# Kernel optimization log

Hardware: AMD Instinct MI355X
Metric: run time of the kernel (lower is better)

The kernel has to match this reference:

```python
import jax, jax.numpy as jnp
import numpy as np

N_NODES = 100000
N_EDGES = 1600000
IN_CH = 32
HID = 128
EDGE_DIM = 16
BN_EPS = 1e-5


def setup_inputs() -> dict:
    key = jax.random.key(0)
    ks = jax.random.split(key, 32)
    f32 = jnp.float32

    def w(k, shape, scale):
        return jax.random.normal(k, shape, dtype=f32) * scale

    inp = {
        'x': w(ks[0], (N_NODES, IN_CH), 1.0),
        'edge_index': jax.random.randint(ks[1], (2, N_EDGES), 0, N_NODES, dtype=jnp.int32),
        'edge_attr': w(ks[2], (N_EDGES, EDGE_DIM), 1.0),
        # layer 0: in=32 -> out=128
        'l0_We': w(ks[3], (EDGE_DIM, IN_CH), 0.1),
        'l0_be': jnp.zeros((IN_CH,), f32),
        'l0_W1': w(ks[4], (IN_CH, HID), 0.1),
        'l0_b1': jnp.zeros((HID,), f32),
        'l0_W2': w(ks[5], (HID, HID), 0.1),
        'l0_b2': jnp.zeros((HID,), f32),
        'l0_gamma': jnp.ones((HID,), f32),
        'l0_beta': jnp.zeros((HID,), f32),
        # layer 1: 128 -> 128
        'l1_We': w(ks[6], (EDGE_DIM, HID), 0.1),
        'l1_be': jnp.zeros((HID,), f32),
        'l1_W1': w(ks[7], (HID, HID), 0.1),
        'l1_b1': jnp.zeros((HID,), f32),
        'l1_W2': w(ks[8], (HID, HID), 0.1),
        'l1_b2': jnp.zeros((HID,), f32),
        'l1_gamma': jnp.ones((HID,), f32),
        'l1_beta': jnp.zeros((HID,), f32),
        # head MLP: hidden -> hidden -> 1
        'head_W1': w(ks[9], (HID, HID), 0.1),
        'head_b1': jnp.zeros((HID,), f32),
        'head_W2': w(ks[10], (HID, 1), 0.1),
        'head_b2': jnp.zeros((1,), f32),
    }
    return inp


def _gnblock(x, src, dst, e, We, be, W1, b1, W2, b2, gamma, beta):
    # GINE-style message passing: gather -> edge message -> scatter-sum
    msg = jax.nn.relu(x[src] + e @ We + be)              # [E, d_in]
    agg = jax.ops.segment_sum(msg, dst, num_segments=N_NODES)  # [N, d_in]
    h = x + agg                                          # GIN combine (eps=0)
    h = jax.nn.relu(h @ W1 + b1) @ W2 + b2               # 2-layer MLP
    # batch norm over the node dimension (use_norm=True)
    mu = jnp.mean(h, axis=0)
    var = jnp.var(h, axis=0)
    h = (h - mu) * jax.lax.rsqrt(var + BN_EPS) * gamma + beta
    return jax.nn.relu(h)


def reference(x, edge_index, edge_attr,
              l0_We, l0_be, l0_W1, l0_b1, l0_W2, l0_b2, l0_gamma, l0_beta,
              l1_We, l1_be, l1_W1, l1_b1, l1_W2, l1_b2, l1_gamma, l1_beta,
              head_W1, head_b1, head_W2, head_b2):
    src, dst = edge_index[0], edge_index[1]
    h = _gnblock(x, src, dst, edge_attr,
                 l0_We, l0_be, l0_W1, l0_b1, l0_W2, l0_b2, l0_gamma, l0_beta)
    h = _gnblock(h, src, dst, edge_attr,
                 l1_We, l1_be, l1_W1, l1_b1, l1_W2, l1_b2, l1_gamma, l1_beta)
    # MLPBlock head + sigmoid -> per-node selection probability [N, 1]
    out = jax.nn.relu(h @ head_W1 + head_b1) @ head_W2 + head_b2
    return jax.nn.sigmoid(out)
```

## Files before the change

### kernel.cpp

```cpp
#include <hip/hip_runtime.h>

#define NN 100000
#define NE 1600000
#define TMAX 193760
#define NRANGES 24220

typedef unsigned int uint32;
typedef unsigned long long ull;
typedef __attribute__((ext_vector_type(8))) short bf16x8;
typedef __attribute__((ext_vector_type(4))) float f32x4;

__device__ __forceinline__ unsigned short f2bf(float f) {
  unsigned int u = __float_as_uint(f);
  unsigned int r = (u + 0x7fffu + ((u >> 16) & 1u)) >> 16;
  return (unsigned short)r;
}
__device__ __forceinline__ float bf2f(unsigned short u) {
  return __uint_as_float(((unsigned int)u) << 16);
}
__device__ __forceinline__ unsigned int pack2(float a, float b) {
  return (unsigned int)f2bf(a) | ((unsigned int)f2bf(b) << 16);
}
__device__ __forceinline__ float row16_sum(float x) {
  x += __int_as_float(__builtin_amdgcn_mov_dpp(__float_as_int(x), 0x128, 0xf, 0xf, false));
  x += __int_as_float(__builtin_amdgcn_mov_dpp(__float_as_int(x), 0x124, 0xf, 0xf, false));
  x += __int_as_float(__builtin_amdgcn_mov_dpp(__float_as_int(x), 0x122, 0xf, 0xf, false));
  x += __int_as_float(__builtin_amdgcn_mov_dpp(__float_as_int(x), 0x121, 0xf, 0xf, false));
  return x;
}

__device__ __forceinline__ void wconv_body(const float* __restrict__ src,
    unsigned short* __restrict__ dst, int K, int N, int b)
{
  const int i = b * 256 + threadIdx.x;
  if (i < K * N) {
    const int n = i / K, k = i - n * K;
    dst[i] = f2bf(src[k * N + n]);
  }
}

__global__ __launch_bounds__(256) void conv_all(
    const float* __restrict__ l0W1, const float* __restrict__ l0W2,
    const float* __restrict__ l1W1, const float* __restrict__ l1W2,
    const float* __restrict__ hW1,  const float* __restrict__ l0We,
    const float* __restrict__ l1We, const float* __restrict__ x,
    unsigned short* __restrict__ W1t0, unsigned short* __restrict__ W2t0,
    unsigned short* __restrict__ W1t1, unsigned short* __restrict__ W2t1,
    unsigned short* __restrict__ hW1t, unsigned short* __restrict__ Wet0,
    unsigned short* __restrict__ Wet1, unsigned short* __restrict__ xb)
{
  int b = blockIdx.x;
  if (b < 16)  { wconv_body(l0W1, W1t0, 32, 128, b); return; }  b -= 16;
  if (b < 64)  { wconv_body(l0W2, W2t0, 128, 128, b); return; } b -= 64;
  if (b < 64)  { wconv_body(l1W1, W1t1, 128, 128, b); return; } b -= 64;
  if (b < 64)  { wconv_body(l1W2, W2t1, 128, 128, b); return; } b -= 64;
  if (b < 64)  { wconv_body(hW1,  hW1t, 128, 128, b); return; } b -= 64;
  if (b < 2)   { wconv_body(l0We, Wet0, 16, 32, b); return; }   b -= 2;
  if (b < 8)   { wconv_body(l1We, Wet1, 16, 128, b); return; }  b -= 8;
  const int i = b * 256 + threadIdx.x;
  if (i * 8 < NN * 32) {
    const float4 a = ((const float4*)x)[i * 2];
    const float4 d = ((const float4*)x)[i * 2 + 1];
    uint4 o;
    o.x = pack2(a.x, a.y); o.y = pack2(a.z, a.w);
    o.z = pack2(d.x, d.y); o.w = pack2(d.z, d.w);
    ((uint4*)xb)[i] = o;
  }
}

__global__ __launch_bounds__(256) void hist_kernel(
    const int* __restrict__ ei, uint32* __restrict__ deg)
{
  const int e = blockIdx.x * 256 + threadIdx.x;
  if (e < NE) atomicAdd(&deg[ei[NE + e]], 1u);
}

__global__ __launch_bounds__(256) void offsets2_kernel(
    const uint32* __restrict__ deg, uint32* __restrict__ toff,
    uint32* __restrict__ eoff, ull* __restrict__ counter)
{
  __shared__ ull s[256];
  __shared__ ull base;
  const int tid = threadIdx.x;
  const int n = blockIdx.x * 256 + tid;
  const uint32 d = (n < NN) ? deg[n] : 0u;
  const uint32 tc = (d + 15u) >> 4;
  const ull v = ((ull)tc << 32) | (ull)d;
  s[tid] = v;
  __syncthreads();
#pragma unroll
  for (int st = 1; st < 256; st <<= 1) {
    ull w = (tid >= st) ? s[tid - st] : 0ull;
    __syncthreads();
    s[tid] += w;
    __syncthreads();
  }
  if (tid == 255) base = atomicAdd(counter, s[255]);
  __syncthreads();
  if (n < NN) {
    const ull t = base + (s[tid] - v);
    toff[n] = (uint32)(t >> 32);
    eoff[n] = (uint32)t;
  }
}

__global__ __launch_bounds__(256) void snode_fill(
    const uint32* __restrict__ toff, const uint32* __restrict__ deg,
    int* __restrict__ snode)
{
  const int n = blockIdx.x * 256 + threadIdx.x;
  if (n < NN) {
    const uint32 t0 = toff[n];
    const uint32 tc = (deg[n] + 15u) >> 4;
    for (uint32 i = 0; i < tc; ++i) snode[t0 + i] = n;
  }
}

template<bool EAB>
__global__ __launch_bounds__(256) void fill_kernel(
    const int* __restrict__ ei, const uint32* __restrict__ eoff,
    uint32* __restrict__ cnt, uint32* __restrict__ srcc,
    unsigned short* __restrict__ eabc, uint32* __restrict__ eidc,
    const float* __restrict__ ea)
{
  const int e = blockIdx.x * 256 + threadIdx.x;
  if (e < NE) {
    const int dst = ei[NE + e];
    const uint32 pos = eoff[dst] + atomicAdd(&cnt[dst], 1u);
    srcc[pos] = (uint32)ei[e];
    if constexpr (EAB) {
      const float4* er = (const float4*)(ea + (size_t)e * 16);
      const float4 p0 = er[0], p1 = er[1], p2 = er[2], p3 = er[3];
      uint4 lo, hi;
      lo.x = pack2(p0.x, p0.y); lo.y = pack2(p0.z, p0.w);
      lo.z = pack2(p1.x, p1.y); lo.w = pack2(p1.z, p1.w);
      hi.x = pack2(p2.x, p2.y); hi.y = pack2(p2.z, p2.w);
      hi.z = pack2(p3.x, p3.y); hi.w = pack2(p3.z, p3.w);
      *(uint4*)&eabc[(size_t)pos * 16]     = lo;
      *(uint4*)&eabc[(size_t)pos * 16 + 8] = hi;
    } else {
      eidc[pos] = (uint32)e;
    }
  }
}

template<int D, int NCT>
__global__ __launch_bounds__(256) void flat_agg2(
    const int* __restrict__ snode, const uint32* __restrict__ toff,
    const uint32* __restrict__ eoff, const uint32* __restrict__ deg,
    const uint32* __restrict__ srcc, const unsigned short* __restrict__ eabc,
    const unsigned short* __restrict__ hsrc,
    const unsigned short* __restrict__ Wet, const float* __restrict__ be,
    const ull* __restrict__ tot, float* __restrict__ agg)
{
  const int tid = threadIdx.x;
  const int wid = tid >> 6;
  const int lane = tid & 63;
  const int c = lane & 15;
  const int g = lane >> 4;
  constexpr bool HALF = (NCT * 16 != D);
  int range, ch0;
  if (HALF) { range = blockIdx.x * 2 + (wid >> 1); ch0 = (wid & 1) * (NCT * 16); }
  else      { range = blockIdx.x * 4 + wid;        ch0 = 0; }
  const int tile0 = range * 8;
  const uint32 ntile = (uint32)((*tot) >> 32);
  if ((uint32)tile0 >= ntile) return;

  bf16x8 wf[NCT];
#pragma unroll
  for (int ct = 0; ct < NCT; ++ct) {
    const int chA = ch0 + (c >> 2) * (NCT * 4) + ct * 4 + (c & 3);
    uint4 u = make_uint4(0u, 0u, 0u, 0u);
    if (g < 2) u = *(const uint4*)&Wet[chA * 16 + g * 8];
    else if (g == 2) u.x = (uint32)f2bf(be[chA]);
    union { uint4 u4; bf16x8 v; } cv; cv.u4 = u;
    wf[ct] = cv.v;
  }

  int sn8 = -1, pk8 = 0, p_ = 0;
  if (lane < 8) {
    sn8 = snode[tile0 + lane];
    if (sn8 >= 0) {
      const uint32 to = toff[sn8], dg = deg[sn8], eo = eoff[sn8];
      const int k = tile0 + lane - (int)to;
      p_ = (int)eo + k * 16;
      int rv = (int)dg - k * 16; if (rv > 16) rv = 16;
      const int fl = (k == 0 ? 1 : 0) |
                     ((k == (int)((dg + 15u) >> 4) - 1) ? 2 : 0);
      pk8 = (rv << 7) | (fl << 12);
    }
  }
  const int p0base = __shfl(p_, 0);
  if (lane < 8 && sn8 >= 0) pk8 |= (p_ - p0base);

  const uint32 sl0 = srcc[(size_t)p0base + lane];
  const uint32 sl1 = srcc[(size_t)p0base + 64 + lane];

  float acc[NCT][4];
#pragma unroll
  for (int ct = 0; ct < NCT; ++ct) {
    acc[ct][0] = 0.f; acc[ct][1] = 0.f; acc[ct][2] = 0.f; acc[ct][3] = 0.f;
  }
  int openNode = -1; bool openFull = false, openClosed = false;

  auto flushOpen = [&](bool storeOK) {
#pragma unroll
    for (int ct = 0; ct < NCT; ++ct)
#pragma unroll
      for (int j = 0; j < 4; ++j)
        acc[ct][j] = row16_sum(acc[ct][j]);
    float4 sv = make_float4(0.f, 0.f, 0.f, 0.f);
#pragma unroll
    for (int ct = 0; ct < NCT; ++ct)
      if (c == ct)
        sv = make_float4(acc[ct][0], acc[ct][1], acc[ct][2], acc[ct][3]);
    if (c < NCT) {
      float* p = &agg[(size_t)openNode * D + ch0 + g * (NCT * 4) + c * 4];
      if (storeOK) {
        *(float4*)p = sv;
      } else {
        atomicAdd(p + 0, sv.x); atomicAdd(p + 1, sv.y);
        atomicAdd(p + 2, sv.z); atomicAdd(p + 3, sv.w);
      }
    }
  };

  auto issue = [&](int t, uint4& afu, uint4& h0, uint4& h1, int& n_, int& mt_) {
    n_ = __shfl(sn8, t);
    mt_ = __shfl(pk8, t);
    const int d0 = mt_ & 127;
    const int rem = (mt_ >> 7) & 31;
    const int idx = d0 + ((c < rem) ? c : 0);
    const uint32 v0 = __shfl(sl0, idx & 63);
    const uint32 v1 = __shfl(sl1, idx & 63);
    const int src = (int)((idx & 64) ? v1 : v0);
    if (g < 2) afu = *(const uint4*)&eabc[((size_t)p0base + idx) * 16 + g * 8];
    h0 = *(const uint4*)&hsrc[(size_t)src * D + ch0 + g * (NCT * 4)];
    if constexpr (NCT == 4)
      h1 = *(const uint4*)&hsrc[(size_t)src * D + ch0 + g * (NCT * 4) + 8];
  };

  auto compute = [&](const uint4 afu, const uint4 h0, const uint4 h1,
                     const int n, const int mt) {
    if (n < 0) return;
    const int rem = (mt >> 7) & 31;
    const int fl = mt >> 12;
    if (n != openNode) {
      if (openNode >= 0) {
        flushOpen(openFull);
#pragma unroll
        for (int ct = 0; ct < NCT; ++ct) {
          acc[ct][0] = 0.f; acc[ct][1] = 0.f;
          acc[ct][2] = 0.f; acc[ct][3] = 0.f;
        }
      }
      openNode = n; openFull = (fl & 1) != 0; openClosed = false;
    }
    if (fl & 2) openClosed = true;
    const float validf = (c < rem) ? 1.0f : 0.0f;
    bf16x8 afv;
    {
      uint4 u = make_uint4(0u, 0u, 0u, 0u);
      if (g < 2) u = afu;
      else if (g == 2) u.x = 0x3f80u;
      union { uint4 u4; bf16x8 v; } cv; cv.u4 = u; afv = cv.v;
    }
#pragma unroll
    for (int ct = 0; ct < NCT; ++ct) {
      f32x4 pre = __builtin_amdgcn_mfma_f32_16x16x32_bf16(
          wf[ct], afv, (f32x4){0.f, 0.f, 0.f, 0.f}, 0, 0, 0);
#pragma unroll
      for (int j = 0; j < 4; ++j) {
        const int ix = ct * 4 + j;
        const uint4 hu = (ix < 8) ? h0 : h1;
        uint32 wv;
        switch ((ix & 7) >> 1) {
          case 0: wv = hu.x; break;
          case 1: wv = hu.y; break;
          case 2: wv = hu.z; break;
          default: wv = hu.w; break;
        }
        const float hvv = bf2f((unsigned short)((ix & 1) ? (wv >> 16) : (wv & 0xffffu)));
        const float m = fmaxf(pre[j] + hvv, 0.f);
        acc[ct][j] = fmaf(validf, m, acc[ct][j]);
      }
    }
  };

  uint4 afA = make_uint4(0,0,0,0), h0A = make_uint4(0,0,0,0), h1A = make_uint4(0,0,0,0);
  uint4 afB = make_uint4(0,0,0,0), h0B = make_uint4(0,0,0,0), h1B = make_uint4(0,0,0,0);
  int nA = -1, mA = 0, nB = -1, mB = 0;

  issue(0, afA, h0A, h1A, nA, mA);
#pragma unroll
  for (int t = 0; t < 8; ++t) {
    if ((t & 1) == 0) {
      if (t < 7) issue(t + 1, afB, h0B, h1B, nB, mB);
      compute(afA, h0A, h1A, nA, mA);
    } else {
      if (t < 7) issue(t + 1, afA, h0A, h1A, nA, mA);
      compute(afB, h0B, h1B, nB, mB);
    }
  }
  if (openNode >= 0) flushOpen(openFull && openClosed);
}

template<int D, int NCT>
__global__ __launch_bounds__(256) void flat_agg_fb(
    const int* __restrict__ snode, const uint32* __restrict__ toff,
    const uint32* __restrict__ eoff, const uint32* __restrict__ deg,
    const uint32* __restrict__ srcc, const uint32* __restrict__ eidc,
    const float* __restrict__ ea, const unsigned short* __restrict__ hsrc,
    const unsigned short* __restrict__ Wet, const float* __restrict__ be,
    const ull* __restrict__ tot, float* __restrict__ agg)
{
  const int tid = threadIdx.x;
  const int wid = tid >> 6;
  const int lane = tid & 63;
  const int c = lane & 15;
  const int g = lane >> 4;
  constexpr bool HALF = (NCT * 16 != D);
  int range, ch0;
  if (HALF) { range = blockIdx.x * 2 + (wid >> 1); ch0 = (wid & 1) * (NCT * 16); }
  else      { range = blockIdx.x * 4 + wid;        ch0 = 0; }
  const int tile0 = range * 8;
  const uint32 ntile = (uint32)((*tot) >> 32);
  if ((uint32)tile0 >= ntile) return;

  bf16x8 wf[NCT];
#pragma unroll
  for (int ct = 0; ct < NCT; ++ct) {
    uint4 u = make_uint4(0u, 0u, 0u, 0u);
    const int ch = ch0 + ct * 16 + c;
    if (g < 2) u = *(const uint4*)&Wet[ch * 16 + g * 8];
    else if (g == 2) u.x = (uint32)f2bf(be[ch]);
    union { uint4 u4; bf16x8 v; } cv; cv.u4 = u;
    wf[ct] = cv.v;
  }

  int sn8 = -1, ps8 = 0, rm8 = 0, fl8 = 0;
  if (lane < 8) {
    sn8 = snode[tile0 + lane];
    if (sn8 >= 0) {
      const uint32 to = toff[sn8], dg = deg[sn8], eo = eoff[sn8];
      const int k = tile0 + lane - (int)to;
      ps8 = (int)eo + k * 16;
      rm8 = (int)dg - k * 16;
      fl8 = (k == 0 ? 1 : 0) | ((k == (int)((dg + 15u) >> 4) - 1) ? 2 : 0);
    }
  }

  float accv[NCT][4];
#pragma unroll
  for (int ct = 0; ct < NCT; ++ct) {
    accv[ct][0] = 0.f; accv[ct][1] = 0.f; accv[ct][2] = 0.f; accv[ct][3] = 0.f;
  }
  int openNode = -1; bool openFull = false, openClosed = false;

  float4 eA0, eA1, eB0, eB1;
  uint2 hxA[NCT], hxB[NCT];
  int nA = -1, rA = 0, fA = 0, nB = -1, rB = 0, fB = 0;

  auto issue = [&](int t, float4& E0, float4& E1, uint2* hx,
                   int& n_, int& r_, int& f_) {
    n_ = __shfl(sn8, t);
    const int p0 = __shfl(ps8, t);
    r_ = __shfl(rm8, t);
    f_ = __shfl(fl8, t);
    const int idx = p0 + ((c < r_) ? c : 0);
    const int e = (int)eidc[idx];
    if (g < 2) {
      E0 = *(const float4*)&ea[(size_t)e * 16 + g * 8];
      E1 = *(const float4*)&ea[(size_t)e * 16 + g * 8 + 4];
    }
    const int sr = (int)srcc[idx];
#pragma unroll
    for (int ct = 0; ct < NCT; ++ct)
      hx[ct] = *(const uint2*)&hsrc[(size_t)sr * D + ch0 + ct * 16 + g * 4];
  };

  auto flushOpen = [&](bool storeOK) {
#pragma unroll
    for (int ct = 0; ct < NCT; ++ct)
#pragma unroll
      for (int j = 0; j < 4; ++j)
        accv[ct][j] = row16_sum(accv[ct][j]);
    float4 sv = make_float4(0.f, 0.f, 0.f, 0.f);
#pragma unroll
    for (int ct = 0; ct < NCT; ++ct)
      if (c == ct)
        sv = make_float4(accv[ct][0], accv[ct][1], accv[ct][2], accv[ct][3]);
    if (c < NCT) {
      float* p = &agg[(size_t)openNode * D + ch0 + c * 16 + g * 4];
      if (storeOK) {
        *(float4*)p = sv;
      } else {
        atomicAdd(p + 0, sv.x); atomicAdd(p + 1, sv.y);
        atomicAdd(p + 2, sv.z); atomicAdd(p + 3, sv.w);
      }
    }
  };

  auto compute = [&](const float4 E0, const float4 E1, const uint2* hx,
                     int n, int r_, int f_) {
    if (n < 0) return;
    if (n != openNode) {
      if (openNode >= 0) {
        flushOpen(openFull);
#pragma unroll
        for (int ct = 0; ct < NCT; ++ct) {
          accv[ct][0] = 0.f; accv[ct][1] = 0.f;
          accv[ct][2] = 0.f; accv[ct][3] = 0.f;
        }
      }
      openNode = n; openFull = (f_ & 1) != 0; openClosed = false;
    }
    if (f_ & 2) openClosed = true;
    const float validf = (c < r_) ? 1.0f : 0.0f;
    bf16x8 afv;
    {
      uint4 u = make_uint4(0u, 0u, 0u, 0u);
      if (g < 2) {
        u.x = pack2(E0.x, E0.y); u.y = pack2(E0.z, E0.w);
        u.z = pack2(E1.x, E1.y); u.w = pack2(E1.z, E1.w);
      } else if (g == 2) u.x = 0x3f80u;
      union { uint4 u4; bf16x8 v; } cv; cv.u4 = u; afv = cv.v;
    }
#pragma unroll
    for (int ct = 0; ct < NCT; ++ct) {
      f32x4 pre = __builtin_amdgcn_mfma_f32_16x16x32_bf16(
          wf[ct], afv, (f32x4){0.f, 0.f, 0.f, 0.f}, 0, 0, 0);
      const float m0 = fmaxf(pre[0] + bf2f((unsigned short)(hx[ct].x & 0xffffu)), 0.f);
      const float m1 = fmaxf(pre[1] + bf2f((unsigned short)(hx[ct].x >> 16)), 0.f);
      const float m2 = fmaxf(pre[2] + bf2f((unsigned short)(hx[ct].y & 0xffffu)), 0.f);
      const float m3 = fmaxf(pre[3] + bf2f((unsigned short)(hx[ct].y >> 16)), 0.f);
      accv[ct][0] = fmaf(validf, m0, accv[ct][0]);
      accv[ct][1] = fmaf(validf, m1, accv[ct][1]);
      accv[ct][2] = fmaf(validf, m2, accv[ct][2]);
      accv[ct][3] = fmaf(validf, m3, accv[ct][3]);
    }
  };

  issue(0, eA0, eA1, hxA, nA, rA, fA);
#pragma unroll
  for (int t = 0; t < 8; ++t) {
    if ((t & 1) == 0) {
      if (t < 7) issue(t + 1, eB0, eB1, hxB, nB, rB, fB);
      compute(eA0, eA1, hxA, nA, rA, fA);
    } else {
      if (t < 7) issue(t + 1, eA0, eA1, hxA, nA, rA, fA);
      compute(eB0, eB1, hxB, nB, rB, fB);
    }
  }
  if (openNode >= 0) flushOpen(openFull && openClosed);
}

template<int DIN, bool ABF16>
__global__ __launch_bounds__(256) void mlp_mfma(
    const float* __restrict__ a32, const unsigned short* __restrict__ abf,
    const float* __restrict__ agg,
    const unsigned short* __restrict__ W1t, const float* __restrict__ b1,
    const unsigned short* __restrict__ W2t, const float* __restrict__ b2,
    float* __restrict__ outp, float* __restrict__ stats, int nChunks)
{
  constexpr int P1 = (DIN == 128) ? 136 : 40;
  constexpr int KS1 = DIN / 32;
  __shared__ __align__(16) unsigned short hin[64 * P1];
  __shared__ __align__(16) unsigned short tls[64 * 136];
  const int tid = threadIdx.x;
  const int w = tid >> 6;
  const int lane = tid & 63;
  const int c = lane & 15, g = lane >> 4;
  const int cw = w * 32;

  bf16x8 B1[2][KS1], B2[2][4];
#pragma unroll
  for (int ct = 0; ct < 2; ++ct)
#pragma unroll
    for (int kk = 0; kk < KS1; ++kk)
      B1[ct][kk] = *(const bf16x8*)&W1t[(cw + ct * 16 + c) * DIN + kk * 32 + g * 8];
#pragma unroll
  for (int ct = 0; ct < 2; ++ct)
#pragma unroll
    for (int kk = 0; kk < 4; ++kk)
      B2[ct][kk] = *(const bf16x8*)&W2t[(cw + ct * 16 + c) * 128 + kk * 32 + g * 8];
  const float b1c0 = b1[cw + c], b1c1 = b1[cw + 16 + c];
  const float b2c0 = b2[cw + c], b2c1 = b2[cw + 16 + c];
  float lsum0 = 0.f, lsum1 = 0.f, lsq0 = 0.f, lsq1 = 0.f;

  for (int chunk = blockIdx.x; chunk < nChunks; chunk += gridDim.x) {
    const int base = chunk * 64;
    if constexpr (DIN == 128) {
#pragma unroll
      for (int p = 0; p < 4; ++p) {
        const int idx = tid + 256 * p;
        const int n = idx >> 4, k8 = idx & 15;
        const int node = base + n;
        uint4 ov = make_uint4(0u, 0u, 0u, 0u);
        if (node < NN) {
          const float4 g0 = *(const float4*)&agg[node * 128 + k8 * 8];
          const float4 g1 = *(const float4*)&agg[node * 128 + k8 * 8 + 4];
          const uint4 hv = *(const uint4*)&abf[node * 128 + k8 * 8];
          ov.x = pack2(bf2f((unsigned short)(hv.x & 0xffffu)) + g0.x,
                       bf2f((unsigned short)(hv.x >> 16)) + g0.y);
          ov.y = pack2(bf2f((unsigned short)(hv.y & 0xffffu)) + g0.z,
                       bf2f((unsigned short)(hv.y >> 16)) + g0.w);
          ov.z = pack2(bf2f((unsigned short)(hv.z & 0xffffu)) + g1.x,
                       bf2f((unsigned short)(hv.z >> 16)) + g1.y);
          ov.w = pack2(bf2f((unsigned short)(hv.w & 0xffffu)) + g1.z,
                       bf2f((unsigned short)(hv.w >> 16)) + g1.w);
        }
        *(uint4*)&hin[n * P1 + k8 * 8] = ov;
      }
    } else {
      const int n = tid >> 2, k8 = tid & 3;
      const int node = base + n;
      uint4 ov = make_uint4(0u, 0u, 0u, 0u);
      if (node < NN) {
        const float4 x0 = *(const float4*)&a32[node * 32 + k8 * 8];
        const float4 x1 = *(const float4*)&a32[node * 32 + k8 * 8 + 4];
        const float4 g0 = *(const float4*)&agg[node * 32 + k8 * 8];
        const float4 g1 = *(const float4*)&agg[node * 32 + k8 * 8 + 4];
        ov.x = pack2(x0.x + g0.x, x0.y + g0.y);
        ov.y = pack2(x0.z + g0.z, x0.w + g0.w);
        ov.z = pack2(x1.x + g1.x, x1.y + g1.y);
        ov.w = pack2(x1.z + g1.z, x1.w + g1.w);
      }
      *(uint4*)&hin[n * P1 + k8 * 8] = ov;
    }
    __syncthreads();
#pragma unroll
    for (int nt = 0; nt < 4; ++nt) {
      bf16x8 af[KS1];
#pragma unroll
      for (int kk = 0; kk < KS1; ++kk)
        af[kk] = *(const bf16x8*)&hin[(nt * 16 + c) * P1 + kk * 32 + g * 8];
      f32x4 acc0 = {0.f, 0.f, 0.f, 0.f}, acc1 = {0.f, 0.f, 0.f, 0.f};
#pragma unroll
      for (int kk = 0; kk < KS1; ++kk) {
        acc0 = __builtin_amdgcn_mfma_f32_16x16x32_bf16(af[kk], B1[0][kk], acc0, 0, 0, 0);
        acc1 = __builtin_amdgcn_mfma_f32_16x16x32_bf16(af[kk], B1[1][kk], acc1, 0, 0, 0);
      }
#pragma unroll
      for (int j = 0; j < 4; ++j) {
        const int row = nt * 16 + g * 4 + j;
        tls[row * 136 + cw + c]      = f2bf(fmaxf(acc0[j] + b1c0, 0.f));
        tls[row * 136 + cw + 16 + c] = f2bf(fmaxf(acc1[j] + b1c1, 0.f));
      }
    }
    __syncthreads();
#pragma unroll
    for (int nt = 0; nt < 4; ++nt) {
      bf16x8 af[4];
#pragma unroll
      for (int kk = 0; kk < 4; ++kk)
        af[kk] = *(const bf16x8*)&tls[(nt * 16 + c) * 136 + kk * 32 + g * 8];
      f32x4 acc0 = {0.f, 0.f, 0.f, 0.f}, acc1 = {0.f, 0.f, 0.f, 0.f};
#pragma unroll
      for (int kk = 0; kk < 4; ++kk) {
        acc0 = __builtin_amdgcn_mfma_f32_16x16x32_bf16(af[kk], B2[0][kk], acc0, 0, 0, 0);
        acc1 = __builtin_amdgcn_mfma_f32_16x16x32_bf16(af[kk], B2[1][kk], acc1, 0, 0, 0);
      }
#pragma unroll
      for (int j = 0; j < 4; ++j) {
        const int node = base + nt * 16 + g * 4 + j;
        if (node < NN) {
          const float v0 = acc0[j] + b2c0;
          const float v1 = acc1[j] + b2c1;
          outp[node * 128 + cw + c] = v0;
          outp[node * 128 + cw + 16 + c] = v1;
          lsum0 += v0; lsq0 += v0 * v0;
          lsum1 += v1; lsq1 += v1 * v1;
        }
      }
    }
  }
  lsum0 += __shfl_xor(lsum0, 16); lsum0 += __shfl_xor(lsum0, 32);
  lsum1 += __shfl_xor(lsum1, 16); lsum1 += __shfl_xor(lsum1, 32);
  lsq0  += __shfl_xor(lsq0, 16);  lsq0  += __shfl_xor(lsq0, 32);
  lsq1  += __shfl_xor(lsq1, 16);  lsq1  += __shfl_xor(lsq1, 32);
  if (lane < 16) {
    atomicAdd(&stats[cw + lane], lsum0);
    atomicAdd(&stats[cw + 16 + lane], lsum1);
    atomicAdd(&stats[128 + cw + lane], lsq0);
    atomicAdd(&stats[128 + cw + 16 + lane], lsq1);
  }
}

__global__ void bn_finalize(float* __restrict__ stats,
                            const float* __restrict__ gamma,
                            const float* __restrict__ beta)
{
  const int cc = threadIdx.x;
  const float inv_n = 1.0f / (float)NN;
  const float mu = stats[cc] * inv_n;
  float var = stats[128 + cc] * inv_n - mu * mu;
  var = fmaxf(var, 0.f);
  const float rs = rsqrtf(var + 1e-5f);
  const float sc = rs * gamma[cc];
  stats[256 + cc] = sc;
  stats[384 + cc] = beta[cc] - mu * sc;
}

__global__ __launch_bounds__(256) void bn_apply_bf16(
    const float* __restrict__ h, const float* __restrict__ stats,
    unsigned short* __restrict__ hb)
{
  const int idx = blockIdx.x * 256 + threadIdx.x;
  const int c4 = (idx & 31) * 4;
  const float4 sc = *(const float4*)&stats[256 + c4];
  const float4 sh = *(const float4*)&stats[384 + c4];
  const float4 v = ((const float4*)h)[idx];
  const float r0 = fmaxf(fmaf(v.x, sc.x, sh.x), 0.f);
  const float r1 = fmaxf(fmaf(v.y, sc.y, sh.y), 0.f);
  const float r2 = fmaxf(fmaf(v.z, sc.z, sh.z), 0.f);
  const float r3 = fmaxf(fmaf(v.w, sc.w, sh.w), 0.f);
  uint2 o;
  o.x = pack2(r0, r1);
  o.y = pack2(r2, r3);
  ((uint2*)hb)[idx] = o;
}

__global__ __launch_bounds__(256) void head_bn(
    const float* __restrict__ hpre, const float* __restrict__ stats,
    const unsigned short* __restrict__ W1t, const float* __restrict__ b1,
    const float* __restrict__ w2, const float* __restrict__ b2,
    float* __restrict__ out, int nChunks)
{
  __shared__ float pl[4][64];
  const int tid = threadIdx.x;
  const int w = tid >> 6;
  const int lane = tid & 63;
  const int c = lane & 15, g = lane >> 4;
  const int cw = w * 32;

  bf16x8 B1[2][4];
#pragma unroll
  for (int ct = 0; ct < 2; ++ct)
#pragma unroll
    for (int kk = 0; kk < 4; ++kk)
      B1[ct][kk] = *(const bf16x8*)&W1t[(cw + ct * 16 + c) * 128 + kk * 32 + g * 8];
  const float b1c0 = b1[cw + c], b1c1 = b1[cw + 16 + c];
  const float w2c0 = w2[cw + c], w2c1 = w2[cw + 16 + c];
  const float b2v = b2[0];
  float4 scq[4][2], shq[4][2];
#pragma unroll
  for (int kk = 0; kk < 4; ++kk) {
    const int cb = kk * 32 + g * 8;
    scq[kk][0] = *(const float4*)&stats[256 + cb];
    scq[kk][1] = *(const float4*)&stats[256 + cb + 4];
    shq[kk][0] = *(const float4*)&stats[384 + cb];
    shq[kk][1] = *(const float4*)&stats[384 + cb + 4];
  }

  for (int chunk = blockIdx.x; chunk < nChunks; chunk += gridDim.x) {
    const int base = chunk * 64;
    float p[4][4];
#pragma unroll
    for (int nt = 0; nt < 4; ++nt) {
      const int node = base + nt * 16 + c;
      bf16x8 af[4];
#pragma unroll
      for (int kk = 0; kk < 4; ++kk) {
        uint4 u = make_uint4(0u, 0u, 0u, 0u);
        if (node < NN) {
          const float4 v0 = *(const float4*)&hpre[(size_t)node * 128 + kk * 32 + g * 8];
          const float4 v1 = *(const float4*)&hpre[(size_t)node * 128 + kk * 32 + g * 8 + 4];
          const float4 s0 = scq[kk][0], s1 = scq[kk][1];
          const float4 h0 = shq[kk][0], h1 = shq[kk][1];
          u.x = pack2(fmaxf(fmaf(v0.x, s0.x, h0.x), 0.f),
                      fmaxf(fmaf(v0.y, s0.y, h0.y), 0.f));
          u.y = pack2(fmaxf(fmaf(v0.z, s0.z, h0.z), 0.f),
                      fmaxf(fmaf(v0.w, s0.w, h0.w), 0.f));
          u.z = pack2(fmaxf(fmaf(v1.x, s1.x, h1.x), 0.f),
                      fmaxf(fmaf(v1.y, s1.y, h1.y), 0.f));
          u.w = pack2(fmaxf(fmaf(v1.z, s1.z, h1.z), 0.f),
                      fmaxf(fmaf(v1.w, s1.w, h1.w), 0.f));
        }
        union { uint4 u4; bf16x8 v; } cv; cv.u4 = u;
        af[kk] = cv.v;
      }
      f32x4 acc0 = {0.f, 0.f, 0.f, 0.f}, acc1 = {0.f, 0.f, 0.f, 0.f};
#pragma unroll
      for (int kk = 0; kk < 4; ++kk) {
        acc0 = __builtin_amdgcn_mfma_f32_16x16x32_bf16(af[kk], B1[0][kk], acc0, 0, 0, 0);
        acc1 = __builtin_amdgcn_mfma_f32_16x16x32_bf16(af[kk], B1[1][kk], acc1, 0, 0, 0);
      }
#pragma unroll
      for (int j = 0; j < 4; ++j)
        p[nt][j] = fmaxf(acc0[j] + b1c0, 0.f) * w2c0 +
                   fmaxf(acc1[j] + b1c1, 0.f) * w2c1;
    }
#pragma unroll
    for (int dd = 1; dd <= 8; dd <<= 1)
#pragma unroll
      for (int nt = 0; nt < 4; ++nt)
#pragma unroll
        for (int j = 0; j < 4; ++j)
          p[nt][j] += __shfl_xor(p[nt][j], dd);
    if (c == 0) {
#pragma unroll
      for (int nt = 0; nt < 4; ++nt)
#pragma unroll
        for (int j = 0; j < 4; ++j)
          pl[w][nt * 16 + g * 4 + j] = p[nt][j];
    }
    __syncthreads();
    if (tid < 64) {
      const int node = base + tid;
      if (node < NN) {
        const float s = pl[0][tid] + pl[1][tid] + pl[2][tid] + pl[3][tid] + b2v;
        out[node] = 1.f / (1.f + expf(-s));
      }
    }
    __syncthreads();
  }
}

extern "C" void kernel_launch(void* const* d_in, const int* in_sizes, int n_in,
                              void* d_out, int out_size, void* d_ws, size_t ws_size,
                              hipStream_t stream)
{
  const float* x    = (const float*)d_in[0];
  const int*   ei   = (const int*)  d_in[1];
  const float* ea   = (const float*)d_in[2];
  const float* l0We = (const float*)d_in[3];
  const float* l0be = (const float*)d_in[4];
  const float* l0W1 = (const float*)d_in[5];
  const float* l0b1 = (const float*)d_in[6];
  const float* l0W2 = (const float*)d_in[7];
  const float* l0b2 = (const float*)d_in[8];
  const float* l0g  = (const float*)d_in[9];
  const float* l0bt = (const float*)d_in[10];
  const float* l1We = (const float*)d_in[11];
  const float* l1be = (const float*)d_in[12];
  const float* l1W1 = (const float*)d_in[13];
  const float* l1b1 = (const float*)d_in[14];
  const float* l1W2 = (const float*)d_in[15];
  const float* l1b2 = (const float*)d_in[16];
  const float* l1g  = (const float*)d_in[17];
  const float* l1bt = (const float*)d_in[18];
  const float* hW1  = (const float*)d_in[19];
  const float* hb1  = (const float*)d_in[20];
  const float* hW2  = (const float*)d_in[21];
  const float* hb2  = (const float*)d_in[22];
  float* out = (float*)d_out;

  float*  A    = (float*)d_ws;
  float*  AGG  = A + (size_t)NN * 128;
  unsigned short* hb = (unsigned short*)(AGG + (size_t)NN * 128);
  unsigned short* xb = hb + (size_t)NN * 128;
  uint32* deg     = (uint32*)(xb + (size_t)NN * 32);
  uint32* cnt     = deg + NN;
  uint32* toff    = cnt + NN;
  uint32* eoff    = toff + NN;
  ull*    counter = (ull*)(eoff + NN);
  int*    snode   = (int*)(counter + 2);
  uint32* srcc    = (uint32*)(snode + TMAX);
  float*  st0     = (float*)(srcc + NE) + 128;
  float*  st1     = st0 + 512;
  unsigned short* W1t0 = (unsigned short*)(st1 + 512);
  unsigned short* W2t0 = W1t0 + 4096;
  unsigned short* W1t1 = W2t0 + 16384;
  unsigned short* W2t1 = W1t1 + 16384;
  unsigned short* hW1t = W2t1 + 16384;
  unsigned short* Wet0 = hW1t + 16384;
  unsigned short* Wet1 = Wet0 + 512;
  unsigned short* eabc = Wet1 + 2048;
  uint32* eidc = (uint32*)eabc;

  const size_t base_need = (size_t)((char*)(Wet1 + 2048) - (char*)d_ws);
  const size_t need_A = base_need + (size_t)NE * 16 * 2;
  const size_t need_B = base_need + (size_t)NE * 4;
  const bool EAB = (ws_size >= need_A);
  if (!EAB && ws_size < need_B) return;

  hipMemsetAsync(deg, 0, (size_t)2 * NN * 4, stream);
  hipMemsetAsync(counter, 0, 16, stream);
  hipMemsetAsync(snode, 0xFF, (size_t)TMAX * 4, stream);
  hipMemsetAsync(st0, 0, 4096, stream);
  hipMemsetAsync(AGG, 0, (size_t)NN * 32 * 4, stream);

  const int nChunks = (NN + 63) / 64;

  conv_all<<<16 + 64 * 4 + 2 + 8 + 1563, 256, 0, stream>>>(
      l0W1, l0W2, l1W1, l1W2, hW1, l0We, l1We, x,
      W1t0, W2t0, W1t1, W2t1, hW1t, Wet0, Wet1, xb);

  hist_kernel<<<(NE + 255) / 256, 256, 0, stream>>>(ei, deg);
  offsets2_kernel<<<(NN + 255) / 256, 256, 0, stream>>>(deg, toff, eoff, counter);
  snode_fill<<<(NN + 255) / 256, 256, 0, stream>>>(toff, deg, snode);
  if (EAB)
    fill_kernel<true><<<(NE + 255) / 256, 256, 0, stream>>>(
        ei, eoff, cnt, srcc, eabc, eidc, ea);
  else
    fill_kernel<false><<<(NE + 255) / 256, 256, 0, stream>>>(
        ei, eoff, cnt, srcc, eabc, eidc, ea);

  if (EAB)
    flat_agg2<32, 2><<<NRANGES / 4, 256, 0, stream>>>(
        snode, toff, eoff, deg, srcc, eabc, xb, Wet0, l0be, counter, AGG);
  else
    flat_agg_fb<32, 2><<<NRANGES / 4, 256, 0, stream>>>(
        snode, toff, eoff, deg, srcc, eidc, ea, xb, Wet0, l0be, counter, AGG);
  mlp_mfma<32, false><<<782, 256, 0, stream>>>(x, (const unsigned short*)nullptr,
      AGG, W1t0, l0b1, W2t0, l0b2, A, st0, nChunks);
  hipMemsetAsync(AGG, 0, (size_t)NN * 128 * 4, stream);
  bn_finalize<<<1, 128, 0, stream>>>(st0, l0g, l0bt);
  bn_apply_bf16<<<(NN * 32) / 256, 256, 0, stream>>>(A, st0, hb);

  if (EAB)
    flat_agg2<128, 4><<<NRANGES / 2, 256, 0, stream>>>(
        snode, toff, eoff, deg, srcc, eabc, hb, Wet1, l1be, counter, AGG);
  else
    flat_agg_fb<128, 4><<<NRANGES / 2, 256, 0, stream>>>(
        snode, toff, eoff, deg, srcc, eidc, ea, hb, Wet1, l1be, counter, AGG);
  mlp_mfma<128, true><<<782, 256, 0, stream>>>((const float*)nullptr, hb,
      AGG, W1t1, l1b1, W2t1, l1b2, A, st1, nChunks);
  bn_finalize<<<1, 128, 0, stream>>>(st1, l1g, l1bt);

  head_bn<<<782, 256, 0, stream>>>(A, st1, hW1t, hb1, hW2, hb2, out, nChunks);
}
```

Measured before the change: 544.0 us.

## Split CSR fill into index scatter plus coalesced gather-convert, deepen agg prefetch

The fused fill kernel scattered 64-byte bf16 edge-attribute rows and source indices to random CSR positions. It is now split in two. The first kernel scatters only the edge id, using the A buffer as scratch. A second kernel walks CSR positions in order, gathers the source index and edge attributes, and writes them coalesced. Separately, the flat_agg2 software pipeline moves from double to triple buffering of issued loads to hide more gather latency, at the cost of an extra kernel launch, an extra index pass and higher register pressure.

```diff
diff --git a/kernel.cpp b/kernel.cpp
--- a/kernel.cpp
+++ b/kernel.cpp
@@ -116,31 +116,50 @@
   }
 }
 
-template<bool EAB>
-__global__ __launch_bounds__(256) void fill_kernel(
+__global__ __launch_bounds__(256) void fill_idx(
+    const int* __restrict__ ei, const uint32* __restrict__ eoff,
+    uint32* __restrict__ cnt, uint32* __restrict__ eidcA)
+{
+  const int e = blockIdx.x * 256 + threadIdx.x;
+  if (e < NE) {
+    const int dst = ei[NE + e];
+    const uint32 pos = eoff[dst] + atomicAdd(&cnt[dst], 1u);
+    eidcA[pos] = (uint32)e;
+  }
+}
+
+__global__ __launch_bounds__(256) void convert_csr(
+    const uint32* __restrict__ eidcA, const int* __restrict__ ei,
+    const float* __restrict__ ea, uint32* __restrict__ srcc,
+    unsigned short* __restrict__ eabc)
+{
+  const int pos = blockIdx.x * 256 + threadIdx.x;
+  if (pos < NE) {
+    const int e = (int)eidcA[pos];
+    srcc[pos] = (uint32)ei[e];
+    const float4* er = (const float4*)(ea + (size_t)e * 16);
+    const float4 p0 = er[0], p1 = er[1], p2 = er[2], p3 = er[3];
+    uint4 lo, hi;
+    lo.x = pack2(p0.x, p0.y); lo.y = pack2(p0.z, p0.w);
+    lo.z = pack2(p1.x, p1.y); lo.w = pack2(p1.z, p1.w);
+    hi.x = pack2(p2.x, p2.y); hi.y = pack2(p2.z, p2.w);
+    hi.z = pack2(p3.x, p3.y); hi.w = pack2(p3.z, p3.w);
+    *(uint4*)&eabc[(size_t)pos * 16]     = lo;
+    *(uint4*)&eabc[(size_t)pos * 16 + 8] = hi;
+  }
+}
+
+__global__ __launch_bounds__(256) void fill_fb(
     const int* __restrict__ ei, const uint32* __restrict__ eoff,
     uint32* __restrict__ cnt, uint32* __restrict__ srcc,
-    unsigned short* __restrict__ eabc, uint32* __restrict__ eidc,
-    const float* __restrict__ ea)
+    uint32* __restrict__ eidc)
 {
   const int e = blockIdx.x * 256 + threadIdx.x;
   if (e < NE) {
     const int dst = ei[NE + e];
     const uint32 pos = eoff[dst] + atomicAdd(&cnt[dst], 1u);
     srcc[pos] = (uint32)ei[e];
-    if constexpr (EAB) {
-      const float4* er = (const float4*)(ea + (size_t)e * 16);
-      const float4 p0 = er[0], p1 = er[1], p2 = er[2], p3 = er[3];
-      uint4 lo, hi;
-      lo.x = pack2(p0.x, p0.y); lo.y = pack2(p0.z, p0.w);
-      lo.z = pack2(p1.x, p1.y); lo.w = pack2(p1.z, p1.w);
-      hi.x = pack2(p2.x, p2.y); hi.y = pack2(p2.z, p2.w);
-      hi.z = pack2(p3.x, p3.y); hi.w = pack2(p3.z, p3.w);
-      *(uint4*)&eabc[(size_t)pos * 16]     = lo;
-      *(uint4*)&eabc[(size_t)pos * 16 + 8] = hi;
-    } else {
-      eidc[pos] = (uint32)e;
-    }
+    eidc[pos] = (uint32)e;
   }
 }
 
@@ -289,19 +308,20 @@
 
   uint4 afA = make_uint4(0,0,0,0), h0A = make_uint4(0,0,0,0), h1A = make_uint4(0,0,0,0);
   uint4 afB = make_uint4(0,0,0,0), h0B = make_uint4(0,0,0,0), h1B = make_uint4(0,0,0,0);
-  int nA = -1, mA = 0, nB = -1, mB = 0;
+  uint4 afC = make_uint4(0,0,0,0), h0C = make_uint4(0,0,0,0), h1C = make_uint4(0,0,0,0);
+  int nA = -1, mA = 0, nB = -1, mB = 0, nC = -1, mC = 0;
 
   issue(0, afA, h0A, h1A, nA, mA);
-#pragma unroll
-  for (int t = 0; t < 8; ++t) {
-    if ((t & 1) == 0) {
-      if (t < 7) issue(t + 1, afB, h0B, h1B, nB, mB);
-      compute(afA, h0A, h1A, nA, mA);
-    } else {
-      if (t < 7) issue(t + 1, afA, h0A, h1A, nA, mA);
-      compute(afB, h0B, h1B, nB, mB);
-    }
-  }
+  issue(1, afB, h0B, h1B, nB, mB);
+  issue(2, afC, h0C, h1C, nC, mC);
+  compute(afA, h0A, h1A, nA, mA); issue(3, afA, h0A, h1A, nA, mA);
+  compute(afB, h0B, h1B, nB, mB); issue(4, afB, h0B, h1B, nB, mB);
+  compute(afC, h0C, h1C, nC, mC); issue(5, afC, h0C, h1C, nC, mC);
+  compute(afA, h0A, h1A, nA, mA); issue(6, afA, h0A, h1A, nA, mA);
+  compute(afB, h0B, h1B, nB, mB); issue(7, afB, h0B, h1B, nB, mB);
+  compute(afC, h0C, h1C, nC, mC);
+  compute(afA, h0A, h1A, nA, mA);
+  compute(afB, h0B, h1B, nB, mB);
   if (openNode >= 0) flushOpen(openFull && openClosed);
 }
 
@@ -767,7 +787,8 @@
   unsigned short* Wet0 = hW1t + 16384;
   unsigned short* Wet1 = Wet0 + 512;
   unsigned short* eabc = Wet1 + 2048;
-  uint32* eidc = (uint32*)eabc;
+  uint32* eidcF = (uint32*)eabc;
+  uint32* eidcA = (uint32*)A;
 
   const size_t base_need = (size_t)((char*)(Wet1 + 2048) - (char*)d_ws);
   const size_t need_A = base_need + (size_t)NE * 16 * 2;
@@ -782,27 +803,28 @@
   hipMemsetAsync(AGG, 0, (size_t)NN * 32 * 4, stream);
 
   const int nChunks = (NN + 63) / 64;
+  const int eBlocks = (NE + 255) / 256;
 
   conv_all<<<16 + 64 * 4 + 2 + 8 + 1563, 256, 0, stream>>>(
       l0W1, l0W2, l1W1, l1W2, hW1, l0We, l1We, x,
       W1t0, W2t0, W1t1, W2t1, hW1t, Wet0, Wet1, xb);
 
-  hist_kernel<<<(NE + 255) / 256, 256, 0, stream>>>(ei, deg);
+  hist_kernel<<<eBlocks, 256, 0, stream>>>(ei, deg);
   offsets2_kernel<<<(NN + 255) / 256, 256, 0, stream>>>(deg, toff, eoff, counter);
   snode_fill<<<(NN + 255) / 256, 256, 0, stream>>>(toff, deg, snode);
-  if (EAB)
-    fill_kernel<true><<<(NE + 255) / 256, 256, 0, stream>>>(
-        ei, eoff, cnt, srcc, eabc, eidc, ea);
-  else
-    fill_kernel<false><<<(NE + 255) / 256, 256, 0, stream>>>(
-        ei, eoff, cnt, srcc, eabc, eidc, ea);
+  if (EAB) {
+    fill_idx<<<eBlocks, 256, 0, stream>>>(ei, eoff, cnt, eidcA);
+    convert_csr<<<eBlocks, 256, 0, stream>>>(eidcA, ei, ea, srcc, eabc);
+  } else {
+    fill_fb<<<eBlocks, 256, 0, stream>>>(ei, eoff, cnt, srcc, eidcF);
+  }
 
   if (EAB)
     flat_agg2<32, 2><<<NRANGES / 4, 256, 0, stream>>>(
         snode, toff, eoff, deg, srcc, eabc, xb, Wet0, l0be, counter, AGG);
   else
     flat_agg_fb<32, 2><<<NRANGES / 4, 256, 0, stream>>>(
-        snode, toff, eoff, deg, srcc, eidc, ea, xb, Wet0, l0be, counter, AGG);
+        snode, toff, eoff, deg, srcc, eidcF, ea, xb, Wet0, l0be, counter, AGG);
   mlp_mfma<32, false><<<782, 256, 0, stream>>>(x, (const unsigned short*)nullptr,
       AGG, W1t0, l0b1, W2t0, l0b2, A, st0, nChunks);
   hipMemsetAsync(AGG, 0, (size_t)NN * 128 * 4, stream);
@@ -814,7 +836,7 @@
         snode, toff, eoff, deg, srcc, eabc, hb, Wet1, l1be, counter, AGG);
   else
     flat_agg_fb<128, 4><<<NRANGES / 2, 256, 0, stream>>>(
-        snode, toff, eoff, deg, srcc, eidc, ea, hb, Wet1, l1be, counter, AGG);
+        snode, toff, eoff, deg, srcc, eidcF, ea, hb, Wet1, l1be, counter, AGG);
   mlp_mfma<128, true><<<782, 256, 0, stream>>>((const float*)nullptr, hb,
       AGG, W1t1, l1b1, W2t1, l1b2, A, st1, nChunks);
   bn_finalize<<<1, 128, 0, stream>>>(st1, l1g, l1bt);
```

After: 585.8 us. +7.7%, slower.
